# Kernel tuning notes

Measured on AMD Instinct MI355X. Metric: run time of the kernel, lower is better.

The kernel has to match this reference:

```python
import jax, jax.numpy as jnp
import numpy as np

EPS = 1e-12  # F.normalize eps

def _normalize(v, axis):
    n = jnp.sqrt(jnp.sum(v * v, axis=axis, keepdims=True))
    return v / jnp.maximum(n, EPS)

def setup_inputs() -> dict:
    key = jax.random.key(0)
    ks = jax.random.split(key, 7)
    N, D, E = 100000, 128, 1600000
    x = jax.random.normal(ks[0], (N, D), dtype=jnp.float32)
    edge_index = jax.random.randint(ks[1], (2, E), 0, N, dtype=jnp.int64)
    s = 1.0 / np.sqrt(D)
    W_l = jax.random.normal(ks[2], (D, D), dtype=jnp.float32) * s
    b_l = jnp.zeros((D,), dtype=jnp.float32)
    W_r = jax.random.normal(ks[3], (D, D), dtype=jnp.float32) * s
    W1 = jax.random.normal(ks[4], (D, 10), dtype=jnp.float32)
    W2 = jax.random.normal(ks[5], (D, 20), dtype=jnp.float32)
    return {"x": x, "edge_index": edge_index, "W_l": W_l, "b_l": b_l,
            "W_r": W_r, "W1": W1, "W2": W2}

def reference(x, edge_index, W_l, b_l, W_r, W1, W2):
    N = x.shape[0]
    src, dst = edge_index[0], edge_index[1]
    # SAGEConv mean aggregation: gather source feats, scatter-mean to targets
    msg = x[src]                                   # [E, D]
    agg = jax.ops.segment_sum(msg, dst, num_segments=N)     # [N, D]
    deg = jax.ops.segment_sum(jnp.ones_like(dst, dtype=x.dtype), dst,
                              num_segments=N)               # [N]
    agg = agg / jnp.maximum(deg, 1.0)[:, None]
    # out = lin_l(agg) + lin_r(x)
    h = agg @ W_l + b_l + x @ W_r                  # [N, D]
    # NormedLinear heads: 10 * norm(h, dim=1) @ norm(W, dim=0)
    hn = _normalize(h, axis=1)
    out1 = 10.0 * (hn @ _normalize(W1, axis=0))
    out2 = 10.0 * (hn @ _normalize(W2, axis=0))
    return (out1, out2, h)
```

## Files before the change

kernel.cpp:

```cpp
#include <hip/hip_runtime.h>
#include <math.h>


typedef __attribute__((ext_vector_type(8))) short s16x8;
typedef __attribute__((ext_vector_type(4))) float f32x4;

#define NBLK 256
#define BLKT 512
#define SH 8
#define BMASK 255
#define CAP 64

static __device__ __forceinline__ unsigned short f2b(float f) {
  unsigned u = __builtin_bit_cast(unsigned, f);
  u += 0x7fff + ((u >> 16) & 1);
  return (unsigned short)(u >> 16);
}
static __device__ __forceinline__ float b2f(unsigned short s) {
  unsigned u = ((unsigned)s) << 16;
  return __builtin_bit_cast(float, u);
}


__global__ __launch_bounds__(BLKT) void scatter_direct(
    const int* __restrict__ ei, int* __restrict__ ebufC,
    int* __restrict__ cellcnt, int* __restrict__ tot,
    int E, int nb, int CH)
{
  __shared__ int cur[512];
  const int b = blockIdx.x;
  const int t = threadIdx.x;
  for (int i = t; i < nb; i += BLKT) cur[i] = 0;
  __syncthreads();
  const int e0 = b * CH, e1 = min(E, e0 + CH);
  const size_t base = (size_t)b * nb;
  for (int e = e0 + t; e < e1; e += BLKT) {
    int src = ei[e];
    int dst = ei[(size_t)E + e];
    int k = dst >> SH;
    int pos = atomicAdd(&cur[k], 1);
    if (pos < CAP)
      ebufC[(base + k) * CAP + pos] = (src << SH) | (dst & BMASK);
  }
  __syncthreads();
  for (int i = t; i < nb; i += BLKT) {
    int c = min(cur[i], CAP);
    cellcnt[base + i] = c;
    if (c) atomicAdd(&tot[i], c);
  }
}

__global__ __launch_bounds__(256) void bucket_scan(
    int* __restrict__ bstart, int nb, int E)
{
  __shared__ int s_sum[256];
  const int t = threadIdx.x;
  const int base = t * 2;
  int v0 = (base < nb) ? bstart[base] : 0;
  int v1 = (base + 1 < nb) ? bstart[base + 1] : 0;
  int s = v0 + v1;
  s_sum[t] = s;
  __syncthreads();
#pragma unroll
  for (int off = 1; off < 256; off <<= 1) {
    int add = (t >= off) ? s_sum[t - off] : 0;
    __syncthreads();
    s_sum[t] += add;
    __syncthreads();
  }
  int run = s_sum[t] - s;
  if (base < nb) bstart[base] = run;
  if (base + 1 < nb) bstart[base + 1] = run + v0;
  if (t == 255) bstart[nb] = E;
}

__global__ __launch_bounds__(256) void csr_finalize_direct(
    const int* __restrict__ ebufC, const int* __restrict__ cellcnt,
    const int* __restrict__ bstart,
    int* __restrict__ offs, int* __restrict__ elist, int N, int E, int nb)
{
  __shared__ int ncnt[256];
  __shared__ int sc[256];
  __shared__ int ncur[256];
  const int k = blockIdx.x;
  const int t = threadIdx.x;
  const int e0 = bstart[k];

  ncnt[t] = 0;
  __syncthreads();
  const int c = cellcnt[(size_t)t * nb + k];
  const int* cell = &ebufC[((size_t)t * nb + k) * CAP];
  for (int i = 0; i < c; ++i)
    atomicAdd(&ncnt[cell[i] & BMASK], 1);
  __syncthreads();
  int v = ncnt[t];
  sc[t] = v;
  __syncthreads();
#pragma unroll
  for (int off = 1; off < 256; off <<= 1) {
    int add = (t >= off) ? sc[t - off] : 0;
    __syncthreads();
    sc[t] += add;
    __syncthreads();
  }
  int ex = e0 + sc[t] - v;
  int node = (k << SH) + t;
  if (node < N) offs[node] = ex;
  ncur[t] = ex;
  if (k == 0 && t == 0) offs[N] = E;
  __syncthreads();
  for (int i = 0; i < c; ++i) {
    int w = cell[i];
    int pos = atomicAdd(&ncur[w & BMASK], 1);
    elist[pos] = w >> SH;
  }
}


__global__ __launch_bounds__(256) void conv_x_kernel(
    const float* __restrict__ x, short* __restrict__ hs, int n8)
{
  int stride = gridDim.x * blockDim.x;
  for (int i = blockIdx.x * blockDim.x + threadIdx.x; i < n8; i += stride) {
    int row = i >> 4, seg = i & 15;
    float4 v0 = ((const float4*)x)[(size_t)row * 32 + seg * 2];
    float4 v1 = ((const float4*)x)[(size_t)row * 32 + seg * 2 + 1];
    s16x8 o;
    o[0] = (short)f2b(v0.x); o[1] = (short)f2b(v0.y);
    o[2] = (short)f2b(v0.z); o[3] = (short)f2b(v0.w);
    o[4] = (short)f2b(v1.x); o[5] = (short)f2b(v1.y);
    o[6] = (short)f2b(v1.z); o[7] = (short)f2b(v1.w);
    *(s16x8*)&hs[(size_t)row * 256 + seg * 8] = o;
  }
}


__global__ __launch_bounds__(256) void agg_gather_b(
    const short* __restrict__ hs_in, short* __restrict__ hs_out,
    const int* __restrict__ offs, const int* __restrict__ elist, int N)
{
  const int lane = threadIdx.x & 63;
  const int row = blockIdx.x * 4 + (threadIdx.x >> 6);
  if (row >= N) return;
  const int qt = lane >> 4;
  const int c  = lane & 15;
  const int start = offs[row], end = offs[row + 1];
  float a[8] = {0.f, 0.f, 0.f, 0.f, 0.f, 0.f, 0.f, 0.f};
  for (int j = start + qt; j < end; j += 4) {
    const s16x8 v = *(const s16x8*)&hs_in[(size_t)elist[j] * 256 + c * 8];
#pragma unroll
    for (int k = 0; k < 8; ++k) a[k] += b2f((unsigned short)v[k]);
  }
#pragma unroll
  for (int k = 0; k < 8; ++k) {
    a[k] += __shfl_xor(a[k], 16);
    a[k] += __shfl_xor(a[k], 32);
  }
  if (qt == 0) {
    float rd = 1.0f / fmaxf((float)(end - start), 1.0f);
    s16x8 o;
#pragma unroll
    for (int k = 0; k < 8; ++k) o[k] = (short)f2b(a[k] * rd);
    *(s16x8*)&hs_out[(size_t)row * 256 + 128 + c * 8] = o;
  }
}

__global__ __launch_bounds__(256) void conv_w_kernel(
    const float* __restrict__ Wl, const float* __restrict__ Wr,
    short* __restrict__ wbT)
{
  int i = blockIdx.x * blockDim.x + threadIdx.x;
  if (i < 128 * 256) {
    int c = i >> 8;
    int k = i & 255;
    float v = (k < 128) ? Wr[(size_t)k * 128 + c] : Wl[(size_t)(k - 128) * 128 + c];
    wbT[i] = (short)f2b(v);
  }
}


__global__ __launch_bounds__(256, 2) void gemm_mfma(
    const short* __restrict__ hs, const short* __restrict__ wbT,
    const float* __restrict__ bl, float* __restrict__ h, int N)
{
  __shared__ short A_s[128][72];
  __shared__ short B_s[128][72];

  const int t = threadIdx.x;
  const int lane = t & 63;
  const int wid = t >> 6;
  const int wr = wid >> 1;
  const int wc = wid & 1;
  const int row0 = blockIdx.x * 128;
  const int l15 = lane & 15;
  const int lhi = lane >> 4;

  f32x4 acc[4][4];
#pragma unroll
  for (int m = 0; m < 4; ++m)
#pragma unroll
    for (int n = 0; n < 4; ++n) acc[m][n] = (f32x4){0.f, 0.f, 0.f, 0.f};

  for (int kc = 0; kc < 4; ++kc) {
    __syncthreads();
#pragma unroll
    for (int uu = 0; uu < 4; ++uu) {
      int u = t + uu * 256;
      int r = u >> 3;
      int s = u & 7;
      s16x8 va = {0, 0, 0, 0, 0, 0, 0, 0};
      int grow = row0 + r;
      if (grow < N)
        va = *(const s16x8*)&hs[(size_t)grow * 256 + kc * 64 + s * 8];
      *(s16x8*)&A_s[r][s * 8] = va;
      s16x8 vb = *(const s16x8*)&wbT[(size_t)r * 256 + kc * 64 + s * 8];
      *(s16x8*)&B_s[r][s * 8] = vb;
    }
    __syncthreads();

#pragma unroll
    for (int ks = 0; ks < 64; ks += 32) {
      const int klo = ks + lhi * 8;
      s16x8 af[4], bf[4];
#pragma unroll
      for (int m = 0; m < 4; ++m)
        af[m] = *(const s16x8*)&A_s[wr * 64 + m * 16 + l15][klo];
#pragma unroll
      for (int n = 0; n < 4; ++n)
        bf[n] = *(const s16x8*)&B_s[wc * 64 + n * 16 + l15][klo];
#pragma unroll
      for (int m = 0; m < 4; ++m)
#pragma unroll
        for (int n = 0; n < 4; ++n)
          acc[m][n] = __builtin_amdgcn_mfma_f32_16x16x32_bf16(
              af[m], bf[n], acc[m][n], 0, 0, 0);
    }
  }

  float bcol[4];
#pragma unroll
  for (int n = 0; n < 4; ++n) bcol[n] = bl[wc * 64 + n * 16 + l15];
#pragma unroll
  for (int m = 0; m < 4; ++m) {
    int grow_base = row0 + wr * 64 + m * 16 + lhi * 4;
#pragma unroll
    for (int r = 0; r < 4; ++r) {
      int grow = grow_base + r;
      if (grow < N) {
#pragma unroll
        for (int n = 0; n < 4; ++n) {
          int col = wc * 64 + n * 16 + l15;
          h[(size_t)grow * 128 + col] = acc[m][n][r] + bcol[n];
        }
      }
    }
  }
}


__global__ __launch_bounds__(256) void head_kernel(
    const float* __restrict__ h, const float* __restrict__ W1,
    const float* __restrict__ W2,
    float* __restrict__ out1, float* __restrict__ out2,
    int N, int c1, int c2)
{
  __shared__ float wc_s[30][132];
  __shared__ float wnorm[30];
  const int nc = c1 + c2;

  for (int i = threadIdx.x; i < nc * 128; i += 256) {
    int j = i >> 7, l = i & 127;
    wc_s[j][l] = (j < c1) ? W1[(size_t)l * c1 + j]
                          : W2[(size_t)l * c2 + (j - c1)];
  }
  __syncthreads();
  if (threadIdx.x < nc) {
    float ss = 0.f;
    for (int l = 0; l < 128; ++l) { float v = wc_s[threadIdx.x][l]; ss += v * v; }
    wnorm[threadIdx.x] = 1.0f / fmaxf(sqrtf(ss), 1e-12f);
  }
  __syncthreads();
  for (int i = threadIdx.x; i < nc * 128; i += 256) {
    int j = i >> 7;
    wc_s[j][i & 127] *= wnorm[j];
  }
  __syncthreads();

  int row = blockIdx.x * 256 + threadIdx.x;
  if (row >= N) return;
  const float4* h4 = (const float4*)(h + (size_t)row * 128);
  float acc[30];
#pragma unroll
  for (int j = 0; j < 30; ++j) acc[j] = 0.f;
  float ss = 0.f;
#pragma unroll 4
  for (int kk = 0; kk < 32; ++kk) {
    float4 v = h4[kk];
    ss += v.x * v.x + v.y * v.y + v.z * v.z + v.w * v.w;
#pragma unroll
    for (int j = 0; j < 30; ++j) {
      const float4 w = *(const float4*)&wc_s[j][kk * 4];
      acc[j] += v.x * w.x + v.y * w.y + v.z * w.z + v.w * w.w;
    }
  }
  float scale = 10.0f / fmaxf(sqrtf(ss), 1e-12f);
#pragma unroll
  for (int j = 0; j < 10; ++j) out1[(size_t)row * 10 + j] = scale * acc[j];
#pragma unroll
  for (int j = 0; j < 20; ++j) out2[(size_t)row * 20 + j] = scale * acc[10 + j];
}


__global__ __launch_bounds__(256) void edge_scatter(
    const float* __restrict__ x, const int* __restrict__ ei,
    float* __restrict__ agg, float* __restrict__ deg, int E)
{
  long long total = (long long)E * 32;
  long long stride = (long long)gridDim.x * blockDim.x;
  for (long long i = (long long)blockIdx.x * blockDim.x + threadIdx.x;
       i < total; i += stride) {
    int e = (int)(i >> 5);
    int c = (int)(i & 31);
    int src = ei[e];
    int dst = ei[(size_t)E + e];
    float4 v = ((const float4*)x)[(size_t)src * 32 + c];
    float* a = agg + (size_t)dst * 128 + c * 4;
    atomicAdd(a + 0, v.x);
    atomicAdd(a + 1, v.y);
    atomicAdd(a + 2, v.z);
    atomicAdd(a + 3, v.w);
    if (c == 0) atomicAdd(deg + dst, 1.0f);
  }
}

#define FMA4(accR, wv, s) { accR[0] += (s) * wv.x; accR[1] += (s) * wv.y; \
                            accR[2] += (s) * wv.z; accR[3] += (s) * wv.w; }

__global__ __launch_bounds__(256, 2) void gemm_h(
    const float* __restrict__ x, const float* __restrict__ Wl,
    const float* __restrict__ bl, const float* __restrict__ Wr,
    const float* __restrict__ degf, float* __restrict__ aggh, int N)
{
  __shared__ float a_s[128][36];
  __shared__ float x_s[128][36];
  __shared__ float wl_s[32][128];
  __shared__ float wr_s[32][128];

  const int t = threadIdx.x;
  const int tx = t & 15;
  const int ty = t >> 4;
  const int row0 = blockIdx.x * 128;

  float acc0[8][4];
  float acc1[8][4];
#pragma unroll
  for (int r = 0; r < 8; ++r)
#pragma unroll
    for (int c = 0; c < 4; ++c) { acc0[r][c] = 0.f; acc1[r][c] = 0.f; }

  for (int kc = 0; kc < 4; ++kc) {
    __syncthreads();
#pragma unroll
    for (int j = 0; j < 4; ++j) {
      int i = t + 256 * j;
      int r = i >> 3;
      int c4 = i & 7;
      int row = row0 + r;
      float4 av = {0.f, 0.f, 0.f, 0.f};
      float4 xv = {0.f, 0.f, 0.f, 0.f};
      if (row < N) {
        float rd = 1.0f / fmaxf(degf[row], 1.0f);
        av = ((const float4*)aggh)[(size_t)row * 32 + kc * 8 + c4];
        av.x *= rd; av.y *= rd; av.z *= rd; av.w *= rd;
        xv = ((const float4*)x)[(size_t)row * 32 + kc * 8 + c4];
      }
      *(float4*)&a_s[r][c4 * 4] = av;
      *(float4*)&x_s[r][c4 * 4] = xv;
    }
#pragma unroll
    for (int j = 0; j < 4; ++j) {
      int i = t + 256 * j;
      int kk = i >> 5;
      int c4 = i & 31;
      ((float4*)wl_s[kk])[c4] = ((const float4*)Wl)[(size_t)(kc * 32 + kk) * 32 + c4];
      ((float4*)wr_s[kk])[c4] = ((const float4*)Wr)[(size_t)(kc * 32 + kk) * 32 + c4];
    }
    __syncthreads();

#pragma unroll
    for (int k4 = 0; k4 < 8; ++k4) {
      float4 wl0[4], wl1[4], wr0[4], wr1[4];
#pragma unroll
      for (int kk = 0; kk < 4; ++kk) {
        int k = k4 * 4 + kk;
        wl0[kk] = *(const float4*)&wl_s[k][tx * 4];
        wl1[kk] = *(const float4*)&wl_s[k][64 + tx * 4];
        wr0[kk] = *(const float4*)&wr_s[k][tx * 4];
        wr1[kk] = *(const float4*)&wr_s[k][64 + tx * 4];
      }
#pragma unroll
      for (int r = 0; r < 8; ++r) {
        int rr = ty + 16 * r;
        float4 a  = *(const float4*)&a_s[rr][k4 * 4];
        float4 xv = *(const float4*)&x_s[rr][k4 * 4];
        FMA4(acc0[r], wl0[0], a.x); FMA4(acc0[r], wl0[1], a.y);
        FMA4(acc0[r], wl0[2], a.z); FMA4(acc0[r], wl0[3], a.w);
        FMA4(acc0[r], wr0[0], xv.x); FMA4(acc0[r], wr0[1], xv.y);
        FMA4(acc0[r], wr0[2], xv.z); FMA4(acc0[r], wr0[3], xv.w);
        FMA4(acc1[r], wl1[0], a.x); FMA4(acc1[r], wl1[1], a.y);
        FMA4(acc1[r], wl1[2], a.z); FMA4(acc1[r], wl1[3], a.w);
        FMA4(acc1[r], wr1[0], xv.x); FMA4(acc1[r], wr1[1], xv.y);
        FMA4(acc1[r], wr1[2], xv.z); FMA4(acc1[r], wr1[3], xv.w);
      }
    }
  }

  float4 b0 = ((const float4*)bl)[tx];
  float4 b1 = ((const float4*)bl)[16 + tx];
#pragma unroll
  for (int r = 0; r < 8; ++r) {
    int row = row0 + ty + 16 * r;
    if (row < N) {
      float4 o0 = { acc0[r][0] + b0.x, acc0[r][1] + b0.y,
                    acc0[r][2] + b0.z, acc0[r][3] + b0.w };
      float4 o1 = { acc1[r][0] + b1.x, acc1[r][1] + b1.y,
                    acc1[r][2] + b1.z, acc1[r][3] + b1.w };
      ((float4*)aggh)[(size_t)row * 32 + tx] = o0;
      ((float4*)aggh)[(size_t)row * 32 + 16 + tx] = o1;
    }
  }
}


extern "C" void kernel_launch(void* const* d_in, const int* in_sizes, int n_in,
                              void* d_out, int out_size, void* d_ws, size_t ws_size,
                              hipStream_t stream)
{
  const float* x  = (const float*)d_in[0];
  const int*   ei = (const int*)d_in[1];
  const float* Wl = (const float*)d_in[2];
  const float* bl = (const float*)d_in[3];
  const float* Wr = (const float*)d_in[4];
  const float* W1 = (const float*)d_in[5];
  const float* W2 = (const float*)d_in[6];

  const int N  = in_sizes[0] / 128;
  const int E  = in_sizes[1] / 2;
  const int c1 = in_sizes[5] / 128;
  const int c2 = in_sizes[6] / 128;
  const int nb = (N + 255) >> SH;
  const int CH = (E + NBLK - 1) / NBLK;

  float* out1 = (float*)d_out;
  float* out2 = out1 + (size_t)N * c1;
  float* h    = out2 + (size_t)N * c2;

  size_t ints = (size_t)NBLK * nb
              + (nb + 1)
              + (N + 1)
              + (size_t)E
              + (size_t)NBLK * nb * CAP;
  ints = (ints + 3) & ~(size_t)3;
  const size_t need = ints * sizeof(int)
                    + (size_t)128 * 256 * sizeof(short);

  if (ws_size >= need && nb <= 512 && CH / nb < CAP / 2) {
    int* cellcnt = (int*)d_ws;
    int* bstart  = cellcnt + (size_t)NBLK * nb;
    int* offs    = bstart + (nb + 1);
    int* elist   = offs + (N + 1);
    int* ebufC   = elist + E;
    short* wbT   = (short*)((int*)d_ws + ints);
    short* hs    = (short*)h;

    hipMemsetAsync(bstart, 0, (size_t)(nb + 1) * sizeof(int), stream);
    conv_x_kernel<<<2048, 256, 0, stream>>>(x, hs, N * 16);
    scatter_direct<<<NBLK, BLKT, 0, stream>>>(ei, ebufC, cellcnt, bstart, E, nb, CH);
    bucket_scan<<<1, 256, 0, stream>>>(bstart, nb, E);
    csr_finalize_direct<<<nb, 256, 0, stream>>>(ebufC, cellcnt, bstart,
                                                offs, elist, N, E, nb);
    agg_gather_b<<<(N + 3) / 4, 256, 0, stream>>>(hs, hs, offs, elist, N);
    conv_w_kernel<<<128, 256, 0, stream>>>(Wl, Wr, wbT);
    gemm_mfma<<<(N + 127) / 128, 256, 0, stream>>>(hs, wbT, bl, h, N);
  } else {
    float* deg = out1;
    hipMemsetAsync(h,   0, (size_t)N * 128 * sizeof(float), stream);
    hipMemsetAsync(deg, 0, (size_t)N * sizeof(float), stream);
    edge_scatter<<<4096, 256, 0, stream>>>(x, ei, h, deg, E);
    gemm_h<<<(N + 127) / 128, 256, 0, stream>>>(x, Wl, bl, Wr, deg, h, N);
  }
  head_kernel<<<(N + 255) / 256, 256, 0, stream>>>(h, W1, W2, out1, out2, N, c1, c2);
}
```

Baseline: 186.2 us.

## Fuse weight conversion and memset into conv_x, prefetch gather loads, raise gemm occupancy

Folds the weight transpose/convert kernel and the bucket-counter memset into extra blocks of the x-conversion kernel, removing two launches. It also software-pipelines the neighbor gather loop so the next row load is issued before the current one is accumulated. The GEMM launch bound changes from 2 to 4 blocks per CU, which may constrain registers and cause spills.

```diff
diff --git a/kernel.cpp b/kernel.cpp
--- a/kernel.cpp
+++ b/kernel.cpp
@@ -118,19 +118,37 @@
 
 
 __global__ __launch_bounds__(256) void conv_x_kernel(
-    const float* __restrict__ x, short* __restrict__ hs, int n8)
-{
-  int stride = gridDim.x * blockDim.x;
-  for (int i = blockIdx.x * blockDim.x + threadIdx.x; i < n8; i += stride) {
-    int row = i >> 4, seg = i & 15;
-    float4 v0 = ((const float4*)x)[(size_t)row * 32 + seg * 2];
-    float4 v1 = ((const float4*)x)[(size_t)row * 32 + seg * 2 + 1];
-    s16x8 o;
-    o[0] = (short)f2b(v0.x); o[1] = (short)f2b(v0.y);
-    o[2] = (short)f2b(v0.z); o[3] = (short)f2b(v0.w);
-    o[4] = (short)f2b(v1.x); o[5] = (short)f2b(v1.y);
-    o[6] = (short)f2b(v1.z); o[7] = (short)f2b(v1.w);
-    *(s16x8*)&hs[(size_t)row * 256 + seg * 8] = o;
+    const float* __restrict__ x, short* __restrict__ hs, int n8,
+    const float* __restrict__ Wl, const float* __restrict__ Wr,
+    short* __restrict__ wbT, int* __restrict__ bstart, int nbp1)
+{
+  const int b = blockIdx.x;
+  if (b < 2048) {
+    const int stride = 2048 * 256;
+    for (int i = b * 256 + threadIdx.x; i < n8; i += stride) {
+      int row = i >> 4, seg = i & 15;
+      float4 v0 = ((const float4*)x)[(size_t)row * 32 + seg * 2];
+      float4 v1 = ((const float4*)x)[(size_t)row * 32 + seg * 2 + 1];
+      s16x8 o;
+      o[0] = (short)f2b(v0.x); o[1] = (short)f2b(v0.y);
+      o[2] = (short)f2b(v0.z); o[3] = (short)f2b(v0.w);
+      o[4] = (short)f2b(v1.x); o[5] = (short)f2b(v1.y);
+      o[6] = (short)f2b(v1.z); o[7] = (short)f2b(v1.w);
+      *(s16x8*)&hs[(size_t)row * 256 + seg * 8] = o;
+    }
+  } else if (b < 2064) {
+    int i0 = (b - 2048) * 2048 + threadIdx.x;
+#pragma unroll
+    for (int u = 0; u < 8; ++u) {
+      int i = i0 + u * 256;
+      int c = i >> 8;
+      int k = i & 255;
+      float v = (k < 128) ? Wr[(size_t)k * 128 + c]
+                          : Wl[(size_t)(k - 128) * 128 + c];
+      wbT[i] = (short)f2b(v);
+    }
+  } else {
+    for (int i = threadIdx.x; i < nbp1; i += 256) bstart[i] = 0;
   }
 }
 
@@ -146,10 +164,20 @@
   const int c  = lane & 15;
   const int start = offs[row], end = offs[row + 1];
   float a[8] = {0.f, 0.f, 0.f, 0.f, 0.f, 0.f, 0.f, 0.f};
-  for (int j = start + qt; j < end; j += 4) {
-    const s16x8 v = *(const s16x8*)&hs_in[(size_t)elist[j] * 256 + c * 8];
-#pragma unroll
-    for (int k = 0; k < 8; ++k) a[k] += b2f((unsigned short)v[k]);
+
+  int j = start + qt;
+  s16x8 v0 = {0, 0, 0, 0, 0, 0, 0, 0};
+  if (j < end)
+    v0 = *(const s16x8*)&hs_in[(size_t)elist[j] * 256 + c * 8];
+  while (j < end) {
+    int j1 = j + 4;
+    s16x8 v1 = {0, 0, 0, 0, 0, 0, 0, 0};
+    if (j1 < end)
+      v1 = *(const s16x8*)&hs_in[(size_t)elist[j1] * 256 + c * 8];
+#pragma unroll
+    for (int k = 0; k < 8; ++k) a[k] += b2f((unsigned short)v0[k]);
+    v0 = v1;
+    j = j1;
   }
 #pragma unroll
   for (int k = 0; k < 8; ++k) {
@@ -165,21 +193,8 @@
   }
 }
 
-__global__ __launch_bounds__(256) void conv_w_kernel(
-    const float* __restrict__ Wl, const float* __restrict__ Wr,
-    short* __restrict__ wbT)
-{
-  int i = blockIdx.x * blockDim.x + threadIdx.x;
-  if (i < 128 * 256) {
-    int c = i >> 8;
-    int k = i & 255;
-    float v = (k < 128) ? Wr[(size_t)k * 128 + c] : Wl[(size_t)(k - 128) * 128 + c];
-    wbT[i] = (short)f2b(v);
-  }
-}
-
-
-__global__ __launch_bounds__(256, 2) void gemm_mfma(
+
+__global__ __launch_bounds__(256, 4) void gemm_mfma(
     const short* __restrict__ hs, const short* __restrict__ wbT,
     const float* __restrict__ bl, float* __restrict__ h, int N)
 {
@@ -473,14 +488,13 @@
     short* wbT   = (short*)((int*)d_ws + ints);
     short* hs    = (short*)h;
 
-    hipMemsetAsync(bstart, 0, (size_t)(nb + 1) * sizeof(int), stream);
-    conv_x_kernel<<<2048, 256, 0, stream>>>(x, hs, N * 16);
+    conv_x_kernel<<<2065, 256, 0, stream>>>(x, hs, N * 16, Wl, Wr, wbT,
+                                            bstart, nb + 1);
     scatter_direct<<<NBLK, BLKT, 0, stream>>>(ei, ebufC, cellcnt, bstart, E, nb, CH);
     bucket_scan<<<1, 256, 0, stream>>>(bstart, nb, E);
     csr_finalize_direct<<<nb, 256, 0, stream>>>(ebufC, cellcnt, bstart,
                                                 offs, elist, N, E, nb);
     agg_gather_b<<<(N + 3) / 4, 256, 0, stream>>>(hs, hs, offs, elist, N);
-    conv_w_kernel<<<128, 256, 0, stream>>>(Wl, Wr, wbT);
     gemm_mfma<<<(N + 127) / 128, 256, 0, stream>>>(hs, wbT, bl, h, N);
   } else {
     float* deg = out1;
```

Result: faster. 172.5 us (-7.4%).
